# Kernel optimization log

Hardware: AMD Instinct MI355X
Metric: run time of the kernel (lower is better)

The kernel has to match this reference:

```python
import jax, jax.numpy as jnp
import numpy as np

GAMMA = 1.0
INF = 1e8  # large finite value standing in for +inf (keeps vjp NaN-free)


def _pairwise_sq_dist(x, y):
    # x: (B, N, d), y: (B, M, d) -> (B, N, M) squared Euclidean distances
    x2 = jnp.sum(x * x, axis=-1)
    y2 = jnp.sum(y * y, axis=-1)
    xy = jnp.einsum('bnd,bmd->bnm', x, y)
    return x2[:, :, None] + y2[:, None, :] - 2.0 * xy


def _soft_dtw(D, gamma=GAMMA):
    # Soft-DTW DP via anti-diagonal wavefront scan.
    # R[i,j] = D[i,j] + softmin(R[i-1,j-1], R[i-1,j], R[i,j-1])
    # softmin(a,b,c) = -gamma * logsumexp(-[a,b,c]/gamma)
    B, N, M = D.shape
    i_idx = jnp.arange(N)

    def step(carry, d):
        r2, r1 = carry  # diagonals d-2 and d-1, each (B, N) indexed by i
        j = d - i_idx  # column index for each row i on diagonal d
        valid = (j >= 0) & (j < M)
        first = (i_idx == 0)[None, :]
        # R[i-1, j-1] lives at index i-1 of diagonal d-2; R[-1,-1] = 0 for (0,0)
        a = jnp.where(first, jnp.where(d == 0, 0.0, INF), jnp.roll(r2, 1, axis=1))
        # R[i-1, j] lives at index i-1 of diagonal d-1
        b = jnp.where(first, INF, jnp.roll(r1, 1, axis=1))
        # R[i, j-1] lives at index i of diagonal d-1
        c = r1
        dv = jnp.take_along_axis(D, jnp.clip(j, 0, M - 1)[None, :, None], axis=2)[:, :, 0]
        sm = -gamma * jax.nn.logsumexp(jnp.stack([-a, -b, -c]) / gamma, axis=0)
        rnew = jnp.where(valid[None, :], dv + sm, INF)
        return (r1, rnew), None

    init = (jnp.full((B, N), INF, D.dtype), jnp.full((B, N), INF, D.dtype))
    (_, rlast), _ = jax.lax.scan(step, init, jnp.arange(N + M - 1))
    # last diagonal (d = N+M-2) holds R[N-1, M-1] at index i = N-1
    return rlast[:, N - 1]


def _sdtw_normalized(x, y):
    # normalize=True: sdtw(x,y) - 0.5*(sdtw(x,x) + sdtw(y,y)); batch all three DPs
    xs = jnp.concatenate([x, x, y], axis=0)
    ys = jnp.concatenate([y, x, y], axis=0)
    r = _soft_dtw(_pairwise_sq_dist(xs, ys))
    B = x.shape[0]
    return r[:B] - 0.5 * (r[B:2 * B] + r[2 * B:])


def setup_inputs() -> dict:
    key = jax.random.key(0)
    k1, k2 = jax.random.split(key)
    outputs = jax.random.normal(k1, (128, 256, 64), dtype=jnp.float32)
    targets = jax.random.normal(k2, (128, 256, 64), dtype=jnp.float32)
    return {"outputs": outputs, "targets": targets}


def reference(outputs, targets):
    # dis_func == 'Soft_DTW' branch: mean(soft-DTW) + 1e-5
    return _sdtw_normalized(outputs, targets).mean() + 1e-5
```

## Files before the change

kernel.cpp:

```cpp
#include <hip/hip_runtime.h>
#include <hip/hip_bf16.h>

#define NSEQ 256
#define DIM 64
#define NB 128
#define NPAIR 384
#define FINF 1e8f
#define LOG2E 1.4426950408889634f
#define LN2 0.6931471805599453f

using f32x4 = __attribute__((ext_vector_type(4))) float;
using s16x8 = __attribute__((ext_vector_type(8))) short;

__device__ __forceinline__ unsigned short bf16u(float f) {
    __hip_bfloat16 h = __float2bfloat16(f);
    return __builtin_bit_cast(unsigned short, h);
}
__device__ __forceinline__ short bf16s(float f) {
    __hip_bfloat16 h = __float2bfloat16(f);
    return __builtin_bit_cast(short, h);
}
__device__ __forceinline__ float min3f(float a, float b, float c) {
    float d; asm("v_min3_f32 %0, %1, %2, %3" : "=v"(d) : "v"(a), "v"(b), "v"(c));
    return d;
}
__device__ __forceinline__ float max3f(float a, float b, float c) {
    float d; asm("v_max3_f32 %0, %1, %2, %3" : "=v"(d) : "v"(a), "v"(b), "v"(c));
    return d;
}

__global__ __launch_bounds__(256, 3)
void dist_kernel(const float* __restrict__ X, const float* __restrict__ Y,
                 unsigned short* __restrict__ S) {
    __shared__ __align__(16) short b_lds[NSEQ * DIM];
    __shared__ __align__(16) short a_lds[128 * DIM];
    __shared__ float a2[128];
    __shared__ float b2[NSEQ];
    unsigned short* sbuf = reinterpret_cast<unsigned short*>(b_lds);

    const int bid = blockIdx.x;
    const int p = bid >> 1;
    const int h = bid & 1;
    const int b = p & (NB - 1);
    const int g = p >> 7;
    const float* Arow = (g == 2 ? Y : X) + (size_t)b * NSEQ * DIM
                        + (size_t)h * 128 * DIM;
    const float* Brow = (g == 1 ? X : Y) + (size_t)b * NSEQ * DIM;

    const int t = threadIdx.x;
    {
        const float4* bv = reinterpret_cast<const float4*>(Brow) + t * (DIM / 4);
        float sb = 0.f;
#pragma unroll
        for (int q = 0; q < 8; ++q) {
            float4 b0 = bv[2 * q], b1 = bv[2 * q + 1];
            sb += b0.x * b0.x + b0.y * b0.y + b0.z * b0.z + b0.w * b0.w
                + b1.x * b1.x + b1.y * b1.y + b1.z * b1.z + b1.w * b1.w;
            s16x8 pb = { bf16s(b0.x), bf16s(b0.y), bf16s(b0.z), bf16s(b0.w),
                         bf16s(b1.x), bf16s(b1.y), bf16s(b1.z), bf16s(b1.w) };
            *reinterpret_cast<s16x8*>(&b_lds[t * DIM + ((q ^ (t & 7)) << 3)]) = pb;
        }
        b2[t] = sb;
    }
    if (t < 128) {
        const float4* av = reinterpret_cast<const float4*>(Arow) + t * (DIM / 4);
        float sa = 0.f;
#pragma unroll
        for (int q = 0; q < 8; ++q) {
            float4 a0 = av[2 * q], a1 = av[2 * q + 1];
            sa += a0.x * a0.x + a0.y * a0.y + a0.z * a0.z + a0.w * a0.w
                + a1.x * a1.x + a1.y * a1.y + a1.z * a1.z + a1.w * a1.w;
            s16x8 pa = { bf16s(a0.x), bf16s(a0.y), bf16s(a0.z), bf16s(a0.w),
                         bf16s(a1.x), bf16s(a1.y), bf16s(a1.z), bf16s(a1.w) };
            *reinterpret_cast<s16x8*>(&a_lds[t * DIM + ((q ^ (t & 7)) << 3)]) = pa;
        }
        a2[t] = sa;
    }
    __syncthreads();

    const int wave = t >> 6;
    const int lane = t & 63;
    const int lrow = lane & 15;
    const int lk   = lane >> 4;

    s16x8 bfr[4][2];
    float bn[4];
#pragma unroll
    for (int ct = 0; ct < 4; ++ct) {
        const int c = 64 * wave + ct * 16 + lrow;
#pragma unroll
        for (int kk = 0; kk < 2; ++kk) {
            const int kb = kk * 4 + lk;
            bfr[ct][kk] = *reinterpret_cast<const s16x8*>(
                &b_lds[c * DIM + ((kb ^ (c & 7)) << 3)]);
        }
        bn[ct] = b2[c];
    }
    __syncthreads();

    const size_t pbase = (size_t)p * (NSEQ * NSEQ);
#pragma unroll 1
    for (int sloc = 0; sloc < 2; ++sloc) {
        const int rl0 = sloc * 64;
        const int r0  = h * 128 + rl0;
        s16x8 afr[4][2];
#pragma unroll
        for (int rt = 0; rt < 4; ++rt) {
            const int rl = rl0 + rt * 16 + lrow;
#pragma unroll
            for (int kk = 0; kk < 2; ++kk) {
                const int kb = kk * 4 + lk;
                afr[rt][kk] = *reinterpret_cast<const s16x8*>(
                    &a_lds[rl * DIM + ((kb ^ (rl & 7)) << 3)]);
            }
        }
#pragma unroll
        for (int ct = 0; ct < 4; ++ct) {
            const int c = 64 * wave + ct * 16 + lrow;
#pragma unroll
            for (int rt = 0; rt < 4; ++rt) {
                f32x4 acc = {0.f, 0.f, 0.f, 0.f};
                acc = __builtin_amdgcn_mfma_f32_16x16x32_bf16(afr[rt][0], bfr[ct][0], acc, 0, 0, 0);
                acc = __builtin_amdgcn_mfma_f32_16x16x32_bf16(afr[rt][1], bfr[ct][1], acc, 0, 0, 0);
#pragma unroll
                for (int jv = 0; jv < 4; ++jv) {
                    const int rloc = rt * 16 + lk * 4 + jv;
                    const float dist = a2[rl0 + rloc] + bn[ct] - 2.f * acc[jv];
                    sbuf[rloc * NSEQ + (c ^ (((rloc >> 2) & 3) << 4))] = bf16u(dist);
                }
            }
        }
        __syncthreads();
        const int sl = lane >> 4;
        const int q  = lane & 15;
#pragma unroll
        for (int gg = 0; gg < 16; ++gg) {
            const int s = 64 * wave + gg * 4 + sl;
            const int il0 = 4 * q;
            const int swz = ((q & 3) << 4);
            const int j0 = (s - (r0 + il0 + 0)) & 255;
            const int j1 = (s - (r0 + il0 + 1)) & 255;
            const int j2 = (s - (r0 + il0 + 2)) & 255;
            const int j3 = (s - (r0 + il0 + 3)) & 255;
            unsigned int e0 = sbuf[(il0 + 0) * NSEQ + (j0 ^ swz)];
            unsigned int e1 = sbuf[(il0 + 1) * NSEQ + (j1 ^ swz)];
            unsigned int e2 = sbuf[(il0 + 2) * NSEQ + (j2 ^ swz)];
            unsigned int e3 = sbuf[(il0 + 3) * NSEQ + (j3 ^ swz)];
            uint2 w;
            w.x = e0 | (e1 << 16);
            w.y = e2 | (e3 << 16);
            *reinterpret_cast<uint2*>(&S[pbase + (size_t)s * NSEQ + r0 + 4 * q]) = w;
        }
        __syncthreads();
    }
}

__global__ __launch_bounds__(256, 2)
void dtw_kernel(const unsigned short* __restrict__ S, float* __restrict__ rout) {
    __shared__ __align__(16) unsigned short sdD[4 * 3 * 2048];
    __shared__ __align__(16) float bndN[4][3][34];
    __shared__ volatile int prog[4];
    __shared__ volatile int rdprog[4];
    const int t = threadIdx.x;
    const int w = t >> 6;
    const int L = t & 63;
    const int p = blockIdx.x;
    const unsigned short* Sp = S + (size_t)p * (NSEQ * NSEQ);
    const int cfirst = 2 * w, clast = 2 * w + 9;
    const int lrow = L >> 3, lcol = L & 7;
    const bool lz = (L == 0);

    if (L == 0) { prog[w] = -1000; rdprog[w] = cfirst - 1; }
    __syncthreads();

    auto stageck = [&](int cc) {
        const int slot = cc % 3;
#pragma unroll
        for (int k = 0; k < 4; ++k) {
            const int row = (32 * cc + 8 * k + lrow) & 255;
            const char* src = (const char*)Sp + row * 512 + w * 128 + lcol * 16;
            __builtin_amdgcn_global_load_lds(
                (const __attribute__((address_space(1))) void*)src,
                (__attribute__((address_space(3))) void*)
                    &sdD[w * 6144 + slot * 2048 + k * 512],
                16, 0, 0);
        }
    };

    stageck(cfirst); stageck(cfirst + 1);

    float s1 = FINF, s2 = FINF, rp = FINF;
    const int finf_bits = __builtin_bit_cast(int, FINF);
    float out_val = 0.f;

    auto stepfn = [&](float dv2, float bt, float btm1) -> float {
        const float bb = lz ? bt : s1;
        const float a  = lz ? btm1 : s2;
        const float m   = min3f(a, bb, rp);
        const float med = __builtin_amdgcn_fmed3f(a, bb, rp);
        const float M   = max3f(a, bb, rp);
        const float x1 = fmaxf(m - med, -126.0f);
        const float x2 = fmaxf(m - M,   -126.0f);
        const float e1 = __builtin_bit_cast(float,
            (int)__builtin_fmaf(x1, 8388608.0f, 1064992212.0f));
        const float e2 = __builtin_bit_cast(float,
            (int)__builtin_fmaf(x2, 8388608.0f, 1064992212.0f));
        const float e = 1.0f + (e1 + e2);
        const float lg = __builtin_fmaf((float)__builtin_bit_cast(int, e),
                                        1.1920929e-7f, -126.94269504f);
        const float rn = (m - lg) + dv2;
        s2 = s1;
        s1 = __builtin_bit_cast(float,
            __builtin_amdgcn_update_dpp(finf_bits, __builtin_bit_cast(int, rn),
                                        0x138 , 0xF, 0xF, false));
        rp = rn;
        return rn;
    };

#pragma unroll 1
    for (int c = cfirst; c <= clast; ++c) {
        if (w < 3) {
            while (rdprog[w + 1] < c - 2) __builtin_amdgcn_s_sleep(2);
        }
        if (w > 0 && c <= 2 * w + 7) {
            while (prog[w - 1] < c) __builtin_amdgcn_s_sleep(2);
        }
        asm volatile("" ::: "memory");
        if (c < clast) asm volatile("s_waitcnt vmcnt(4)" ::: "memory");
        else           asm volatile("s_waitcnt vmcnt(0)" ::: "memory");

        float dvv[32];
        {
            const unsigned short* db = &sdD[w * 6144 + (c % 3) * 2048 + L];
#pragma unroll
            for (int u = 0; u < 32; ++u)
                dvv[u] = __builtin_bit_cast(float,
                             (unsigned)db[u * 64] << 16) * LOG2E;
        }
        float bwf[32], carA, carB;
        if (w == 0) {
#pragma unroll
            for (int u = 0; u < 32; ++u) bwf[u] = FINF;
            carA = FINF;
            carB = (c == 0) ? 0.f : FINF;
        } else {
            const float* bs = &bndN[w][c % 3][0];
            carB = bs[0];
            carA = bs[1];
#pragma unroll
            for (int u = 0; u < 32; ++u) bwf[u] = bs[2 + u];
        }
        if (c + 2 <= clast) stageck(c + 2);

        float rb[32];
        rb[0] = stepfn(dvv[0], carA, carB);
        rb[1] = stepfn(dvv[1], bwf[0], carA);
#pragma unroll
        for (int u = 2; u < 32; ++u)
            rb[u] = stepfn(dvv[u], bwf[u - 1], bwf[u - 2]);

        if (w < 3) {
            if (L == 63) {
                float* bd = &bndN[w + 1][c % 3][0];
#pragma unroll
                for (int u = 0; u < 32; ++u) bd[2 + u] = rb[u];
                float* bd2 = &bndN[w + 1][(c + 1) % 3][0];
                bd2[0] = rb[30];
                bd2[1] = rb[31];
            }
            asm volatile("s_waitcnt lgkmcnt(0)" ::: "memory");
            if (L == 63) prog[w] = c;
        } else if (c == 15 && L == 63) {
            out_val = rb[30];
        }
        asm volatile("" ::: "memory");
        if (w > 0 && L == 0) rdprog[w] = c;
    }

    if (w == 3 && L == 63) rout[p] = out_val * LN2;
}

__global__ void reduce_kernel(const float* __restrict__ rr, float* __restrict__ out) {
    const int t = threadIdx.x;
    float v = rr[t] - 0.5f * (rr[t + 128] + rr[t + 256]);
#pragma unroll
    for (int o = 32; o > 0; o >>= 1) v += __shfl_down(v, o);
    __shared__ float sred[2];
    if ((t & 63) == 0) sred[t >> 6] = v;
    __syncthreads();
    if (t == 0) out[0] = (sred[0] + sred[1]) * (1.f / 128.f) + 1e-5f;
}

extern "C" void kernel_launch(void* const* d_in, const int* in_sizes, int n_in,
                              void* d_out, int out_size, void* d_ws, size_t ws_size,
                              hipStream_t stream) {
    const float* X = (const float*)d_in[0];
    const float* Y = (const float*)d_in[1];
    float* out = (float*)d_out;

    const size_t dbytes = (size_t)NPAIR * NSEQ * NSEQ * sizeof(unsigned short);
    const size_t need = dbytes + (size_t)NPAIR * sizeof(float);
    if (ws_size < need) {
        hipMemsetAsync(d_out, 0x7f, sizeof(float), stream);
        return;
    }
    unsigned short* Sws = (unsigned short*)d_ws;
    float* rws = (float*)((char*)d_ws + dbytes);

    dist_kernel<<<2 * NPAIR, 256, 0, stream>>>(X, Y, Sws);
    dtw_kernel<<<NPAIR, 256, 0, stream>>>(Sws, rws);
    reduce_kernel<<<1, 128, 0, stream>>>(rws, out);
}
```

Measured before the change: 88.99 us.

## Store distance matrix row-major and load per-lane diagonals directly into registers

The distance kernel now writes its LDS tile straight out in row-major order with vectorized copies, dropping the skewed diagonal transpose on store. The DTW kernel removes its LDS staging through async global-to-LDS loads and instead has each lane read its own row's 32 consecutive values into registers, double-buffered across chunk pairs so loads overlap the recurrence. The workspace gets a 128-byte guard offset so the shifted, possibly out-of-range reads at the band edges stay inside the allocation, and launch bounds drop to one block per SIMD. The trade-off is strided, uncoalesced global loads per lane and higher register pressure in exchange for a cheaper store path and no LDS copies.

```diff
diff --git a/kernel.cpp b/kernel.cpp
--- a/kernel.cpp
+++ b/kernel.cpp
@@ -131,33 +131,21 @@
             }
         }
         __syncthreads();
-        const int sl = lane >> 4;
-        const int q  = lane & 15;
 #pragma unroll
         for (int gg = 0; gg < 16; ++gg) {
-            const int s = 64 * wave + gg * 4 + sl;
-            const int il0 = 4 * q;
-            const int swz = ((q & 3) << 4);
-            const int j0 = (s - (r0 + il0 + 0)) & 255;
-            const int j1 = (s - (r0 + il0 + 1)) & 255;
-            const int j2 = (s - (r0 + il0 + 2)) & 255;
-            const int j3 = (s - (r0 + il0 + 3)) & 255;
-            unsigned int e0 = sbuf[(il0 + 0) * NSEQ + (j0 ^ swz)];
-            unsigned int e1 = sbuf[(il0 + 1) * NSEQ + (j1 ^ swz)];
-            unsigned int e2 = sbuf[(il0 + 2) * NSEQ + (j2 ^ swz)];
-            unsigned int e3 = sbuf[(il0 + 3) * NSEQ + (j3 ^ swz)];
-            uint2 w;
-            w.x = e0 | (e1 << 16);
-            w.y = e2 | (e3 << 16);
-            *reinterpret_cast<uint2*>(&S[pbase + (size_t)s * NSEQ + r0 + 4 * q]) = w;
+            const int row = wave * 16 + gg;
+            const int swz = ((row >> 2) & 3) << 4;
+            uint2 v = *reinterpret_cast<const uint2*>(
+                &sbuf[row * NSEQ + ((4 * lane) ^ swz)]);
+            *reinterpret_cast<uint2*>(
+                &S[pbase + (size_t)(r0 + row) * NSEQ + 4 * lane]) = v;
         }
         __syncthreads();
     }
 }
 
-__global__ __launch_bounds__(256, 2)
+__global__ __launch_bounds__(256, 1)
 void dtw_kernel(const unsigned short* __restrict__ S, float* __restrict__ rout) {
-    __shared__ __align__(16) unsigned short sdD[4 * 3 * 2048];
     __shared__ __align__(16) float bndN[4][3][34];
     __shared__ volatile int prog[4];
     __shared__ volatile int rdprog[4];
@@ -165,29 +153,19 @@
     const int w = t >> 6;
     const int L = t & 63;
     const int p = blockIdx.x;
-    const unsigned short* Sp = S + (size_t)p * (NSEQ * NSEQ);
+    const unsigned short* myrow =
+        S + (size_t)p * (NSEQ * NSEQ) + (size_t)(64 * w + L) * NSEQ;
     const int cfirst = 2 * w, clast = 2 * w + 9;
-    const int lrow = L >> 3, lcol = L & 7;
     const bool lz = (L == 0);
 
     if (L == 0) { prog[w] = -1000; rdprog[w] = cfirst - 1; }
     __syncthreads();
 
-    auto stageck = [&](int cc) {
-        const int slot = cc % 3;
-#pragma unroll
-        for (int k = 0; k < 4; ++k) {
-            const int row = (32 * cc + 8 * k + lrow) & 255;
-            const char* src = (const char*)Sp + row * 512 + w * 128 + lcol * 16;
-            __builtin_amdgcn_global_load_lds(
-                (const __attribute__((address_space(1))) void*)src,
-                (__attribute__((address_space(3))) void*)
-                    &sdD[w * 6144 + slot * 2048 + k * 512],
-                16, 0, 0);
-        }
-    };
-
-    stageck(cfirst); stageck(cfirst + 1);
+    auto loadD = [&](unsigned* buf, int c) {
+        const unsigned short* src = myrow + (32 * c - 64 * w - L);
+#pragma unroll
+        for (int u = 0; u < 32; ++u) buf[u] = src[u];
+    };
 
     float s1 = FINF, s2 = FINF, rp = FINF;
     const int finf_bits = __builtin_bit_cast(int, FINF);
@@ -217,8 +195,7 @@
         return rn;
     };
 
-#pragma unroll 1
-    for (int c = cfirst; c <= clast; ++c) {
+    auto polls = [&](int c) {
         if (w < 3) {
             while (rdprog[w + 1] < c - 2) __builtin_amdgcn_s_sleep(2);
         }
@@ -226,17 +203,9 @@
             while (prog[w - 1] < c) __builtin_amdgcn_s_sleep(2);
         }
         asm volatile("" ::: "memory");
-        if (c < clast) asm volatile("s_waitcnt vmcnt(4)" ::: "memory");
-        else           asm volatile("s_waitcnt vmcnt(0)" ::: "memory");
-
-        float dvv[32];
-        {
-            const unsigned short* db = &sdD[w * 6144 + (c % 3) * 2048 + L];
-#pragma unroll
-            for (int u = 0; u < 32; ++u)
-                dvv[u] = __builtin_bit_cast(float,
-                             (unsigned)db[u * 64] << 16) * LOG2E;
-        }
+    };
+
+    auto process = [&](int c, const unsigned* dbuf) {
         float bwf[32], carA, carB;
         if (w == 0) {
 #pragma unroll
@@ -250,14 +219,15 @@
 #pragma unroll
             for (int u = 0; u < 32; ++u) bwf[u] = bs[2 + u];
         }
-        if (c + 2 <= clast) stageck(c + 2);
-
         float rb[32];
-        rb[0] = stepfn(dvv[0], carA, carB);
-        rb[1] = stepfn(dvv[1], bwf[0], carA);
+        rb[0] = stepfn(__builtin_bit_cast(float, dbuf[0] << 16) * LOG2E,
+                       carA, carB);
+        rb[1] = stepfn(__builtin_bit_cast(float, dbuf[1] << 16) * LOG2E,
+                       bwf[0], carA);
 #pragma unroll
         for (int u = 2; u < 32; ++u)
-            rb[u] = stepfn(dvv[u], bwf[u - 1], bwf[u - 2]);
+            rb[u] = stepfn(__builtin_bit_cast(float, dbuf[u] << 16) * LOG2E,
+                           bwf[u - 1], bwf[u - 2]);
 
         if (w < 3) {
             if (L == 63) {
@@ -275,6 +245,19 @@
         }
         asm volatile("" ::: "memory");
         if (w > 0 && L == 0) rdprog[w] = c;
+    };
+
+    unsigned dA[32], dB[32];
+    loadD(dA, cfirst);
+
+#pragma unroll 1
+    for (int cb = cfirst; cb <= clast; cb += 2) {
+        polls(cb);
+        loadD(dB, cb + 1);
+        process(cb, dA);
+        polls(cb + 1);
+        if (cb + 2 <= clast) loadD(dA, cb + 2);
+        process(cb + 1, dB);
     }
 
     if (w == 3 && L == 63) rout[p] = out_val * LN2;
@@ -299,13 +282,13 @@
     float* out = (float*)d_out;
 
     const size_t dbytes = (size_t)NPAIR * NSEQ * NSEQ * sizeof(unsigned short);
-    const size_t need = dbytes + (size_t)NPAIR * sizeof(float);
+    const size_t need = 128 + dbytes + 128 + (size_t)NPAIR * sizeof(float);
     if (ws_size < need) {
         hipMemsetAsync(d_out, 0x7f, sizeof(float), stream);
         return;
     }
-    unsigned short* Sws = (unsigned short*)d_ws;
-    float* rws = (float*)((char*)d_ws + dbytes);
+    unsigned short* Sws = (unsigned short*)d_ws + 64;
+    float* rws = (float*)((char*)d_ws + 128 + dbytes + 128);
 
     dist_kernel<<<2 * NPAIR, 256, 0, stream>>>(X, Y, Sws);
     dtw_kernel<<<NPAIR, 256, 0, stream>>>(Sws, rws);
```

Result: slower. 105.7 us (+18.8%).
